# Kernel tuning notes

Hardware: AMD Instinct MI355X
Metric: run time of the kernel (lower is better)

## Reference

```python
import jax, jax.numpy as jnp
import numpy as np

HIDDEN = 4096
N_HEADS = 32
N_KV_HEADS = 8
HEAD_DIM = HIDDEN // N_HEADS  # 128
N_KV_GROUPS = N_HEADS // N_KV_HEADS  # 4
SEQ = 2048
BSZ = 1
ROPE_THETA = 10000.0


def _rope_cos_sin(seqlen, head_dim, dtype):
    # freqs_cis = polar(1, outer(t, theta^{-2i/d})) -> cos/sin tables [S, hd/2]
    inv_freq = 1.0 / (ROPE_THETA ** (jnp.arange(0, head_dim, 2, dtype=jnp.float32) / head_dim))
    t = jnp.arange(seqlen, dtype=jnp.float32)
    freqs = jnp.outer(t, inv_freq)  # [S, hd/2]
    return jnp.cos(freqs).astype(dtype), jnp.sin(freqs).astype(dtype)


def _apply_rotary(x, cos, sin):
    # x: [B, S, H, hd]. Torch code pairs (x[:hd/2], x[hd/2:]) as (real, imag):
    # out = concat(x1*cos - x2*sin, x1*sin + x2*cos)
    half = x.shape[-1] // 2
    x1, x2 = x[..., :half], x[..., half:]
    c = cos[None, :, None, :]  # [1, S, 1, hd/2]
    s = sin[None, :, None, :]
    return jnp.concatenate([x1 * c - x2 * s, x1 * s + x2 * c], axis=-1)


def setup_inputs() -> dict:
    key = jax.random.key(0)
    k1, k2, k3 = jax.random.split(key, 3)
    hidden_states = jax.random.normal(k1, (BSZ, SEQ, HIDDEN), dtype=jnp.float32)
    w_qkv = jax.random.normal(k2, (HIDDEN, (N_HEADS + 2 * N_KV_HEADS) * HEAD_DIM), dtype=jnp.float32) * 0.02
    w_o = jax.random.normal(k3, (HIDDEN, HIDDEN), dtype=jnp.float32) * 0.02
    # HF-style additive causal mask [1, 1, S, S]
    causal = jnp.tril(jnp.ones((SEQ, SEQ), dtype=bool))
    attention_mask = jnp.where(causal, 0.0, -1e9).astype(jnp.float32)[None, None]
    return {"hidden_states": hidden_states, "w_qkv": w_qkv, "w_o": w_o,
            "attention_mask": attention_mask}


def reference(hidden_states, w_qkv, w_o, attention_mask):
    bsz, seqlen, _ = hidden_states.shape
    # fused (dequantized) QKV projection
    xqkv = jnp.einsum('bsh,hd->bsd', hidden_states, w_qkv)
    xqkv = xqkv.reshape(bsz, seqlen, N_HEADS + 2 * N_KV_HEADS, HEAD_DIM)
    xq = xqkv[:, :, :N_HEADS]                      # [B, S, 32, 128]
    xk = xqkv[:, :, N_HEADS:N_HEADS + N_KV_HEADS]  # [B, S, 8, 128]
    xv = xqkv[:, :, -N_KV_HEADS:]                  # [B, S, 8, 128]

    cos, sin = _rope_cos_sin(seqlen, HEAD_DIM, hidden_states.dtype)
    xq = _apply_rotary(xq, cos, sin)
    xk = _apply_rotary(xk, cos, sin)

    # GQA: repeat_interleave kv heads along head dim
    keys = jnp.repeat(xk, N_KV_GROUPS, axis=2)    # [B, S, 32, 128]
    values = jnp.repeat(xv, N_KV_GROUPS, axis=2)

    q = xq.transpose(0, 2, 1, 3)   # [B, H, S, D]
    k = keys.transpose(0, 2, 1, 3)
    v = values.transpose(0, 2, 1, 3)

    scores = jnp.einsum('bhqd,bhkd->bhqk', q, k) / np.sqrt(HEAD_DIM)
    scores = scores + attention_mask
    probs = jax.nn.softmax(scores.astype(jnp.float32), axis=-1).astype(q.dtype)
    out = jnp.einsum('bhqk,bhkd->bhqd', probs, v)
    attention_weight = out.transpose(0, 2, 1, 3).reshape(bsz, seqlen, -1)
    attn_output = jnp.einsum('bsh,ho->bso', attention_weight, w_o)
    return attn_output
```

## Files before the change

### kernel.cpp

```cpp
#include <hip/hip_runtime.h>
#include <stdint.h>

typedef unsigned short u16;
typedef __bf16 bf8 __attribute__((ext_vector_type(8)));
typedef float f32x4 __attribute__((ext_vector_type(4)));

#define SEQ 2048
#define HIDDEN 4096
#define DQKV 6144
#define HD 128

#define GLOAD_LDS16(g, l)                                                            \
    __builtin_amdgcn_global_load_lds((const __attribute__((address_space(1))) void*)(g), \
                                     (__attribute__((address_space(3))) void*)(l), 16, 0, 0)

__device__ __forceinline__ u16 f2bf(float f) {
    union { float f; unsigned u; } v{f};
    unsigned r = (v.u + 0x7fff + ((v.u >> 16) & 1)) >> 16;
    return (u16)r;
}
__device__ __forceinline__ float bf2f(u16 b) {
    union { unsigned u; float f; } v;
    v.u = ((unsigned)b) << 16;
    return v.f;
}

__global__ void prep_kernel(const float* __restrict__ hs,
                            const float* __restrict__ wqkv,
                            const float* __restrict__ wo,
                            u16* __restrict__ Hbf,
                            u16* __restrict__ WqkvT,
                            u16* __restrict__ WoT) {
    __shared__ u16 tile[64][65];
    int b = blockIdx.x;
    const int tid = threadIdx.x;
    if (b < 8192) {
        int i = (b * 256 + tid) * 4;
        float4 v = *(const float4*)(hs + i);
        u16 o[4] = {f2bf(v.x), f2bf(v.y), f2bf(v.z), f2bf(v.w)};
        *(uint2*)(Hbf + i) = *(uint2*)o;
        return;
    }
    const float* in;
    u16* out;
    int K, N;
    if (b < 14336) { b -= 8192;  in = wqkv; out = WqkvT; K = HIDDEN; N = DQKV; }
    else           { b -= 14336; in = wo;   out = WoT;   K = HIDDEN; N = HIDDEN; }
    const int tn = N >> 6;
    const int bk = b / tn, bn = b % tn;
    const int k0 = bk * 64, n0 = bn * 64;
    const int c = tid & 63, r0 = tid >> 6;
#pragma unroll
    for (int r = r0; r < 64; r += 4)
        tile[r][c] = f2bf(in[(size_t)(k0 + r) * N + n0 + c]);
    __syncthreads();
#pragma unroll
    for (int r = r0; r < 64; r += 4)
        out[(size_t)(n0 + r) * K + k0 + c] = tile[c][r];
}

__global__ void rope_tv_kernel(u16* __restrict__ x, u16* __restrict__ vt) {
    __shared__ u16 tile[64][65];
    int b = blockIdx.x;
    const int tid = threadIdx.x;
    if (b < 20480) {
        const int row = b / 10, hg = b % 10;
        const int head = hg * 4 + (tid >> 6), j = tid & 63;
        u16* p = x + (size_t)row * DQKV + head * HD + j;
        float x1 = bf2f(p[0]), x2 = bf2f(p[64]);
        float inv = exp2f(-(float)j * 0.20762050593045952f);
        float s, c;
        sincosf((float)row * inv, &s, &c);
        p[0] = f2bf(x1 * c - x2 * s);
        p[64] = f2bf(x1 * s + x2 * c);
        return;
    }
    b -= 20480;
    const int h = b >> 6;
    const int t = b & 63;
    const int s0 = (t >> 1) * 64, d0 = (t & 1) * 64;
    const int c = tid & 63, r0 = tid >> 6;
    const u16* src = x + (40 + h) * HD + d0;
#pragma unroll
    for (int r = r0; r < 64; r += 4)
        tile[r][c] = src[(size_t)(s0 + r) * DQKV + c];
    __syncthreads();
    u16* dst = vt + ((size_t)h * HD + d0) * SEQ + s0;
#pragma unroll
    for (int r = r0; r < 64; r += 4)
        dst[(size_t)r * SEQ + c] = tile[c][r];
}

template <int BM, int BN, int MODE>
__global__ __launch_bounds__(512, 2) void gemm8p_kernel(const u16* __restrict__ A,
                                                        const u16* __restrict__ BT,
                                                        u16* __restrict__ Cbf,
                                                        float* __restrict__ Cf) {
    constexpr int WM = BM / 32;
    constexpr int WN = BN / 64;
    constexpr int MP = WM / 4;
    constexpr int NLA = BM / 64, NLB = BN / 64, NL = NLA + NLB;
    constexpr int NBN = ((MODE == 0) ? DQKV : HIDDEN) / BN;
    constexpr int NBM = SEQ / BM;
    constexpr int CSTR = (MODE == 0) ? DQKV : HIDDEN;
    constexpr int NT = 64;
    static_assert(NBM * NBN == 256, "grid must be exactly 256 blocks");
    __shared__ __align__(16) u16 lds[2][(BM + BN) * 64];

    const int tid = threadIdx.x;
    const int w = tid >> 6, l = tid & 63, l15 = l & 15, q4 = l >> 4;
    const int wm = w >> 2, wn = w & 3;

    const int xcd = blockIdx.x & 7, wi = blockIdx.x >> 3;
    int bm, bn;
    if constexpr (NBN == 32) {
        bm = (xcd >> 2) * 4 + (wi >> 3);
        bn = (xcd & 3) * 8 + (wi & 7);
    } else {
        bm = (xcd & 3) * 4 + (wi >> 3);
        bn = (xcd >> 2) * 8 + (wi & 7);
    }

    const int srow = tid >> 3;
    const int scol = ((tid & 7) ^ ((tid >> 3) & 7)) << 4;
    const char* spA[NLA];
    const char* spB[NLB];
#pragma unroll
    for (int L = 0; L < NLA; ++L)
        spA[L] = (const char*)(A + (size_t)(bm * BM + L * 64 + srow) * 4096) + scol;
#pragma unroll
    for (int L = 0; L < NLB; ++L)
        spB[L] = (const char*)(BT + (size_t)(bn * BN + L * 64 + srow) * 4096) + scol;

#define STG_A(L, tt, b) GLOAD_LDS16(spA[L] + (size_t)(tt) * 128, &lds[b][(L) * 4096 + w * 512])
#define STG_B(L, tt, b) GLOAD_LDS16(spB[L] + (size_t)(tt) * 128, &lds[b][BM * 64 + (L) * 4096 + w * 512])

#pragma unroll
    for (int L = 0; L < NLA; ++L) STG_A(L, 0, 0);
#pragma unroll
    for (int L = 0; L < NLB; ++L) STG_B(L, 0, 0);
#pragma unroll
    for (int L = 0; L < NLA; ++L) STG_A(L, 1, 1);
#pragma unroll
    for (int L = 0; L < NLB; ++L) STG_B(L, 1, 1);
    if constexpr (NL == 7) asm volatile("s_waitcnt vmcnt(7)" ::: "memory");
    else                   asm volatile("s_waitcnt vmcnt(6)" ::: "memory");
    asm volatile("s_barrier" ::: "memory");

    const int c0x = (q4 * 16) ^ ((l15 & 7) << 4);
    const int c1x = c0x ^ 64;

    f32x4 acc[WM][WN] = {};
    bf8 breg[WN][2];

#pragma unroll 1
    for (int t = 0; t < NT; ++t) {
        const int cur = t & 1;
        const char* ldsA = (const char*)&lds[cur][0];
        const char* ldsB = ldsA + BM * 128;
#pragma unroll
        for (int p = 0; p < 4; ++p) {
            if (p == 1 && t < NT - 2) {
#pragma unroll
                for (int L = 0; L < NLB; ++L) STG_B(L, t + 2, cur);
            }
            if constexpr (BM == 256) {
                if (p == 2 && t < NT - 2) {
                    STG_A(0, t + 2, cur);
                    STG_A(2, t + 2, cur);
                }
            }
            bf8 areg[MP][2];
#pragma unroll
            for (int j = 0; j < MP; ++j) {
                const char* rp = ldsA + (wm * (BM / 2) + (p * MP + j) * 16 + l15) * 128;
                areg[j][0] = *(const bf8*)(rp + c0x);
                areg[j][1] = *(const bf8*)(rp + c1x);
            }
            if (p == 0) {
#pragma unroll
                for (int nf = 0; nf < WN; ++nf) {
                    const char* rp = ldsB + (wn * (WN * 16) + nf * 16 + l15) * 128;
                    breg[nf][0] = *(const bf8*)(rp + c0x);
                    breg[nf][1] = *(const bf8*)(rp + c1x);
                }
            }
            asm volatile("s_barrier" ::: "memory");
            asm volatile("s_waitcnt lgkmcnt(0)" ::: "memory");
            __builtin_amdgcn_s_setprio(1);
#pragma unroll
            for (int j = 0; j < MP; ++j)
#pragma unroll
                for (int nf = 0; nf < WN; ++nf)
#pragma unroll
                    for (int ks = 0; ks < 2; ++ks)
                        acc[p * MP + j][nf] = __builtin_amdgcn_mfma_f32_16x16x32_bf16(
                            areg[j][ks], breg[nf][ks], acc[p * MP + j][nf], 0, 0, 0);
            __builtin_amdgcn_s_setprio(0);
            asm volatile("s_barrier" ::: "memory");
        }
        if (t < NT - 2) {
            if constexpr (BM == 256) { STG_A(1, t + 2, cur); STG_A(3, t + 2, cur); }
            else                     { STG_A(0, t + 2, cur); STG_A(1, t + 2, cur); }
            if constexpr (NL == 7) asm volatile("s_waitcnt vmcnt(7)" ::: "memory");
            else                   asm volatile("s_waitcnt vmcnt(6)" ::: "memory");
        } else if (t == NT - 2) {
            asm volatile("s_waitcnt vmcnt(0)" ::: "memory");
        }
        asm volatile("s_barrier" ::: "memory");
    }
#undef STG_A
#undef STG_B

    const int rowb = bm * BM + wm * (BM / 2);
    const int colb = bn * BN + wn * (WN * 16);
#pragma unroll
    for (int mf = 0; mf < WM; ++mf)
#pragma unroll
        for (int nf = 0; nf < WN; ++nf)
#pragma unroll
            for (int r = 0; r < 4; ++r) {
                const int row = rowb + mf * 16 + q4 * 4 + r;
                const int col = colb + nf * 16 + l15;
                if constexpr (MODE == 0)
                    Cbf[(size_t)row * CSTR + col] = f2bf(acc[mf][nf][r]);
                else
                    Cf[(size_t)row * CSTR + col] = acc[mf][nf][r];
            }
}

#define PSTR 72
__global__ __launch_bounds__(256) void attn_kernel(const u16* __restrict__ xqkv,
                                                   const u16* __restrict__ vt,
                                                   u16* __restrict__ aw) {
    __shared__ __align__(16) u16 sm[16384 + 128 * PSTR];
    const int tid = threadIdx.x, w = tid >> 6, l = tid & 63, l15 = l & 15, q4 = l >> 4;
    const int qh = blockIdx.x & 31;
    const int qslot = blockIdx.x >> 5;
    const int qt = (qslot < 8) ? qslot : 23 - qslot;
    const int kh = qh >> 2;

    {
        const u16* gq = xqkv + (size_t)(qt * 128 + (l >> 2)) * DQKV + qh * HD + w * 32 + (l & 3) * 8;
#pragma unroll
        for (int i = 0; i < 8; ++i)
            GLOAD_LDS16(gq + (size_t)i * 16 * DQKV, &sm[w * 4096 + i * 512]);
    }
    __syncthreads();
    bf8 qf[4][2];
#pragma unroll
    for (int ks = 0; ks < 4; ++ks)
#pragma unroll
        for (int mt = 0; mt < 2; ++mt)
            qf[ks][mt] = *(const bf8*)&sm[ks * 4096 + (w * 32 + mt * 16 + l15) * 32 + q4 * 8];
    __syncthreads();

    f32x4 O[2][8] = {};
    float plrow[2][4] = {};

    u16* ldsK = sm;
    u16* ldsV = sm + 8192;
    u16* ldsP = sm + 16384;
    const int nkt = 2 * qt + 2;
    const float cs = 0.12751744f;

    const int sr8 = l >> 3;
    const int sc8 = (l & 7) ^ sr8;
    const u16* gk_base = xqkv + (size_t)((w >> 1) * 32 + sr8) * DQKV + (32 + kh) * HD + (w & 1) * 64 + sc8 * 8;
    u16* ldsK_dst = ldsK + (w & 1) * 4096 + (w >> 1) * 2048;
    const u16* gv_base = vt + ((size_t)kh * HD + w * 32 + sr8) * SEQ + sc8 * 8;
    u16* ldsV_dst = ldsV + w * 2048;

    const int cswz = (q4 ^ (l15 & 7)) << 4;
    const char* Kb = (const char*)ldsK;
    const char* Vb = (const char*)ldsV;

    for (int kt = 0; kt < nkt; ++kt) {
        {
            const u16* gk = gk_base + (size_t)(kt * 64) * DQKV;
#pragma unroll
            for (int i = 0; i < 4; ++i)
                GLOAD_LDS16(gk + (size_t)i * 8 * DQKV, ldsK_dst + i * 512);
        }
        {
            const u16* gv = gv_base + kt * 64;
#pragma unroll
            for (int i = 0; i < 4; ++i)
                GLOAD_LDS16(gv + (size_t)i * 8 * SEQ, ldsV_dst + i * 512);
        }
        __syncthreads();

        f32x4 S[2][4] = {};
#pragma unroll
        for (int ks = 0; ks < 4; ++ks) {
            bf8 kf[4];
#pragma unroll
            for (int nt = 0; nt < 4; ++nt)
                kf[nt] = *(const bf8*)(Kb + (ks >> 1) * 8192 + (nt * 16 + l15) * 128
                                       + (cswz ^ ((ks & 1) << 6)));
#pragma unroll
            for (int mt = 0; mt < 2; ++mt)
#pragma unroll
                for (int nt = 0; nt < 4; ++nt)
                    S[mt][nt] = __builtin_amdgcn_mfma_f32_16x16x32_bf16(qf[ks][mt], kf[nt], S[mt][nt], 0, 0, 0);
        }

        const bool domask = (kt >= 2 * qt);
#pragma unroll
        for (int mt = 0; mt < 2; ++mt)
#pragma unroll
            for (int r = 0; r < 4; ++r) {
                const int row = qt * 128 + w * 32 + mt * 16 + q4 * 4 + r;
#pragma unroll
                for (int nt = 0; nt < 4; ++nt) {
                    float t = S[mt][nt][r] * cs;
                    if (domask && (kt * 64 + nt * 16 + l15 > row)) t = -1e30f;
                    float p = exp2f(t);
                    plrow[mt][r] += p;
                    ldsP[(w * 32 + mt * 16 + q4 * 4 + r) * PSTR + nt * 16 + l15] = f2bf(p);
                }
            }

#pragma unroll
        for (int pk = 0; pk < 2; ++pk) {
            bf8 pf[2], vf[8];
#pragma unroll
            for (int mt = 0; mt < 2; ++mt)
                pf[mt] = *(const bf8*)&ldsP[(w * 32 + mt * 16 + l15) * PSTR + pk * 32 + q4 * 8];
#pragma unroll
            for (int nt = 0; nt < 8; ++nt)
                vf[nt] = *(const bf8*)(Vb + (nt * 16 + l15) * 128 + (cswz ^ (pk << 6)));
#pragma unroll
            for (int mt = 0; mt < 2; ++mt)
#pragma unroll
                for (int nt = 0; nt < 8; ++nt)
                    O[mt][nt] = __builtin_amdgcn_mfma_f32_16x16x32_bf16(pf[mt], vf[nt], O[mt][nt], 0, 0, 0);
        }
        __syncthreads();
    }

#pragma unroll
    for (int mt = 0; mt < 2; ++mt)
#pragma unroll
        for (int r = 0; r < 4; ++r) {
            float ls = plrow[mt][r];
#pragma unroll
            for (int off = 1; off <= 8; off <<= 1)
                ls += __shfl_xor(ls, off, 64);
            const float linv = 1.0f / ls;
            const int row = qt * 128 + w * 32 + mt * 16 + q4 * 4 + r;
#pragma unroll
            for (int nt = 0; nt < 8; ++nt)
                aw[(size_t)row * 4096 + qh * HD + nt * 16 + l15] = f2bf(O[mt][nt][r] * linv);
        }
}


extern "C" void kernel_launch(void* const* d_in, const int* in_sizes, int n_in,
                              void* d_out, int out_size, void* d_ws, size_t ws_size,
                              hipStream_t stream) {
    const float* hs = (const float*)d_in[0];
    const float* wqkv = (const float*)d_in[1];
    const float* wo = (const float*)d_in[2];
    float* out = (float*)d_out;

    char* ws = (char*)d_ws;
    const size_t oHbf = 0;
    const size_t oWqkvT = oHbf + (size_t)SEQ * HIDDEN * 2;
    const size_t oWoT = oWqkvT + (size_t)DQKV * HIDDEN * 2;
    const size_t oXQKV = oWoT + (size_t)HIDDEN * HIDDEN * 2;
    const size_t oVT = oXQKV + (size_t)SEQ * DQKV * 2;
    const size_t oAW = oVT + (size_t)8 * HD * SEQ * 2;
    const size_t total = oAW + (size_t)SEQ * HIDDEN * 2;
    if (ws_size < total) return;

    u16* Hbf = (u16*)(ws + oHbf);
    u16* WqkvT = (u16*)(ws + oWqkvT);
    u16* WoT = (u16*)(ws + oWoT);
    u16* XQKV = (u16*)(ws + oXQKV);
    u16* VT = (u16*)(ws + oVT);
    u16* AW = (u16*)(ws + oAW);

    prep_kernel<<<18432, 256, 0, stream>>>(hs, wqkv, wo, Hbf, WqkvT, WoT);
    gemm8p_kernel<256, 192, 0><<<256, 512, 0, stream>>>(Hbf, WqkvT, XQKV, nullptr);
    rope_tv_kernel<<<20992, 256, 0, stream>>>(XQKV, VT);
    attn_kernel<<<512, 256, 0, stream>>>(XQKV, VT, AW);
    gemm8p_kernel<128, 256, 1><<<256, 512, 0, stream>>>(AW, WoT, nullptr, out);
}
```

Before: 508.9 us.

## Double-buffer K/V tiles in attention and swizzle the P scratch layout

The attention loop now keeps two K and two V buffers in LDS. It prefetches the next key tile with global-to-LDS loads while the current tile is being computed, and drops one of the two barriers per iteration. The padded P staging buffer is replaced by an XOR-swizzled 128-byte-row layout, which is meant to avoid LDS bank conflicts without the padding. LDS use per block rises to about 80 KB, which may reduce how many blocks fit on a CU at once.

```diff
diff --git a/kernel.cpp b/kernel.cpp
--- a/kernel.cpp
+++ b/kernel.cpp
@@ -229,11 +229,10 @@
             }
 }
 
-#define PSTR 72
 __global__ __launch_bounds__(256) void attn_kernel(const u16* __restrict__ xqkv,
                                                    const u16* __restrict__ vt,
                                                    u16* __restrict__ aw) {
-    __shared__ __align__(16) u16 sm[16384 + 128 * PSTR];
+    __shared__ __align__(16) u16 sm[40960];
     const int tid = threadIdx.x, w = tid >> 6, l = tid & 63, l15 = l & 15, q4 = l >> 4;
     const int qh = blockIdx.x & 31;
     const int qslot = blockIdx.x >> 5;
@@ -258,37 +257,45 @@
     f32x4 O[2][8] = {};
     float plrow[2][4] = {};
 
-    u16* ldsK = sm;
-    u16* ldsV = sm + 8192;
-    u16* ldsP = sm + 16384;
+    u16* smK = sm;
+    u16* smV = sm + 16384;
+    char* Pb = (char*)(sm + 32768);
     const int nkt = 2 * qt + 2;
     const float cs = 0.12751744f;
 
     const int sr8 = l >> 3;
     const int sc8 = (l & 7) ^ sr8;
     const u16* gk_base = xqkv + (size_t)((w >> 1) * 32 + sr8) * DQKV + (32 + kh) * HD + (w & 1) * 64 + sc8 * 8;
-    u16* ldsK_dst = ldsK + (w & 1) * 4096 + (w >> 1) * 2048;
+    const int kdst = (w & 1) * 4096 + (w >> 1) * 2048;
     const u16* gv_base = vt + ((size_t)kh * HD + w * 32 + sr8) * SEQ + sc8 * 8;
-    u16* ldsV_dst = ldsV + w * 2048;
+    const int vdst = w * 2048;
 
     const int cswz = (q4 ^ (l15 & 7)) << 4;
-    const char* Kb = (const char*)ldsK;
-    const char* Vb = (const char*)ldsV;
+
+    {
+#pragma unroll
+        for (int i = 0; i < 4; ++i)
+            GLOAD_LDS16(gk_base + (size_t)i * 8 * DQKV, smK + kdst + i * 512);
+#pragma unroll
+        for (int i = 0; i < 4; ++i)
+            GLOAD_LDS16(gv_base + (size_t)i * 8 * SEQ, smV + vdst + i * 512);
+    }
 
     for (int kt = 0; kt < nkt; ++kt) {
-        {
-            const u16* gk = gk_base + (size_t)(kt * 64) * DQKV;
+        __syncthreads();
+        if (kt + 1 < nkt) {
+            const int nxt = (kt + 1) & 1;
+            const u16* gk = gk_base + (size_t)((kt + 1) * 64) * DQKV;
 #pragma unroll
             for (int i = 0; i < 4; ++i)
-                GLOAD_LDS16(gk + (size_t)i * 8 * DQKV, ldsK_dst + i * 512);
-        }
-        {
-            const u16* gv = gv_base + kt * 64;
+                GLOAD_LDS16(gk + (size_t)i * 8 * DQKV, smK + nxt * 8192 + kdst + i * 512);
+            const u16* gv = gv_base + (kt + 1) * 64;
 #pragma unroll
             for (int i = 0; i < 4; ++i)
-                GLOAD_LDS16(gv + (size_t)i * 8 * SEQ, ldsV_dst + i * 512);
-        }
-        __syncthreads();
+                GLOAD_LDS16(gv + (size_t)i * 8 * SEQ, smV + nxt * 8192 + vdst + i * 512);
+        }
+        const char* Kb = (const char*)(smK + (kt & 1) * 8192);
+        const char* Vb = (const char*)(smV + (kt & 1) * 8192);
 
         f32x4 S[2][4] = {};
 #pragma unroll
@@ -310,14 +317,16 @@
         for (int mt = 0; mt < 2; ++mt)
 #pragma unroll
             for (int r = 0; r < 4; ++r) {
-                const int row = qt * 128 + w * 32 + mt * 16 + q4 * 4 + r;
+                const int prow = w * 32 + mt * 16 + q4 * 4 + r;
+                const int row = qt * 128 + prow;
+                const int rsw = (prow & 7) << 4;
 #pragma unroll
                 for (int nt = 0; nt < 4; ++nt) {
                     float t = S[mt][nt][r] * cs;
                     if (domask && (kt * 64 + nt * 16 + l15 > row)) t = -1e30f;
                     float p = exp2f(t);
                     plrow[mt][r] += p;
-                    ldsP[(w * 32 + mt * 16 + q4 * 4 + r) * PSTR + nt * 16 + l15] = f2bf(p);
+                    *(u16*)(Pb + prow * 128 + ((((nt * 16 + l15) * 2)) ^ rsw)) = f2bf(p);
                 }
             }
 
@@ -325,8 +334,10 @@
         for (int pk = 0; pk < 2; ++pk) {
             bf8 pf[2], vf[8];
 #pragma unroll
-            for (int mt = 0; mt < 2; ++mt)
-                pf[mt] = *(const bf8*)&ldsP[(w * 32 + mt * 16 + l15) * PSTR + pk * 32 + q4 * 8];
+            for (int mt = 0; mt < 2; ++mt) {
+                const int prow = w * 32 + mt * 16 + l15;
+                pf[mt] = *(const bf8*)(Pb + prow * 128 + ((pk * 64 + q4 * 16) ^ ((l15 & 7) << 4)));
+            }
 #pragma unroll
             for (int nt = 0; nt < 8; ++nt)
                 vf[nt] = *(const bf8*)(Vb + (nt * 16 + l15) * 128 + (cswz ^ (pk << 6)));
@@ -336,7 +347,6 @@
                 for (int nt = 0; nt < 8; ++nt)
                     O[mt][nt] = __builtin_amdgcn_mfma_f32_16x16x32_bf16(pf[mt], vf[nt], O[mt][nt], 0, 0, 0);
         }
-        __syncthreads();
     }
 
 #pragma unroll
```

Result: faster. 494.6 us (-2.8%).
